# Performance work log

Measured on AMD Instinct MI355X. Metric: run time of the kernel, lower is better.

Reference implementation:

```python
import jax, jax.numpy as jnp
import numpy as np

B, IN, OUT, LAT = 8192, 256, 256, 128

def setup_inputs() -> dict:
    key = jax.random.key(0)
    ks = jax.random.split(key, 6)
    s = 0.05
    return {
        "x": jax.random.normal(ks[0], (B, IN), dtype=jnp.float32),
        "latent": jax.random.normal(ks[1], (B, LAT), dtype=jnp.float32),
        "Ww": jax.random.normal(ks[2], (LAT, IN * OUT), dtype=jnp.float32) * s,
        "bw": jax.random.normal(ks[3], (IN * OUT,), dtype=jnp.float32) * s,
        "Wb": jax.random.normal(ks[4], (LAT, OUT), dtype=jnp.float32) * s,
        "bb": jax.random.normal(ks[5], (OUT,), dtype=jnp.float32) * s,
    }

def reference(x, latent, Ww, bw, Wb, bb):
    lead = x.shape[:-1]
    x2 = x.reshape(-1, x.shape[-1])            # [B, in]
    l2 = latent.reshape(-1, latent.shape[-1])  # [B, lat]
    # per-sample weight: [B, in, out]
    weight = (l2 @ Ww + bw).reshape(-1, IN, OUT)
    # per-sample bias: [B, out]
    bias = l2 @ Wb + bb
    out = jnp.einsum('bi,bio->bo', x2, weight) + bias
    return out.reshape(*lead, OUT)
```

## Files before the change

### kernel.cpp

```cpp
#include <hip/hip_runtime.h>
#include <cstdint>
#include <cstddef>

#define BATCH  8192
#define IN_N   256
#define OUT_N  256
#define LAT_N  128
#define SLABS  129
#define KT     (SLABS * IN_N)
#define KT16   (KT / 16)
#define SPLITK 4

typedef _Float16 h8 __attribute__((ext_vector_type(8)));
typedef _Float16 h4 __attribute__((ext_vector_type(4)));
typedef float    f16v __attribute__((ext_vector_type(16)));
typedef float    f4v  __attribute__((ext_vector_type(4)));

#define WS_BP    0
#define WS_XH    16908288
#define WS_LT    21102592
#define WS_PARTS 23216128

__global__ void k_transpose(const float* __restrict__ Ww, const float* __restrict__ bw,
                            _Float16* __restrict__ Bp) {
    __shared__ float tile[64][65];
    const int k0 = blockIdx.x * 64;
    const int o0 = blockIdx.y * 64;
    const int t  = threadIdx.x;
    const int c  = t & 63, r0 = t >> 6;
#pragma unroll
    for (int j = 0; j < 16; ++j) {
        int r = r0 + 4 * j;
        int k = k0 + r;
        float v;
        if (k < LAT_N * IN_N) v = Ww[(size_t)k * 256 + o0 + c];
        else                  v = bw[(size_t)(k - LAT_N * IN_N) * 256 + o0 + c];
        tile[r][c] = v;
    }
    __syncthreads();
    const int tl = t & 31, st = t >> 5;
    const int kt_l = st >> 1, nt_l = st & 1;
    const int nt   = blockIdx.y * 2 + nt_l;
    const int kt16 = blockIdx.x * 4 + kt_l;
    _Float16* dst = Bp + ((size_t)(nt * KT16 + kt16) * 64) * 8;
#pragma unroll
    for (int kh = 0; kh < 2; ++kh) {
        h8 v;
#pragma unroll
        for (int h = 0; h < 8; ++h)
            v[h] = (_Float16)tile[kt_l * 16 + kh * 8 + h][nt_l * 32 + tl];
        *(h8*)(dst + (size_t)(kh * 32 + tl) * 8) = v;
    }
}

__global__ void k_convert(const float* __restrict__ x, const float* __restrict__ latent,
                          _Float16* __restrict__ Xh, _Float16* __restrict__ LT) {
    const int bid = blockIdx.x;
    if (bid < 2048) {
        int i = (bid * 256 + threadIdx.x) * 4;
        float4 v = *(const float4*)(x + i);
        h4 o;
        o[0] = (_Float16)v.x; o[1] = (_Float16)v.y;
        o[2] = (_Float16)v.z; o[3] = (_Float16)v.w;
        *(h4*)(Xh + i) = o;
    } else if (bid < 2048 + 4096) {
        int i = (bid - 2048) * 256 + threadIdx.x;
        int b = i >> 7, l = i & 127;
        LT[(size_t)l * BATCH + b] = (_Float16)latent[i];
    } else {
        int b = (bid - 2048 - 4096) * 256 + threadIdx.x;
        LT[(size_t)LAT_N * BATCH + b] = (_Float16)1.0f;
    }
}

__global__ void k_bias(const float* __restrict__ latent, const float* __restrict__ Wb,
                       const float* __restrict__ bb, float* __restrict__ part0) {
    __shared__ float lat[8][128];
    const int b0 = blockIdx.x * 8;
    const int t = threadIdx.x;
#pragma unroll
    for (int j = 0; j < 4; ++j) {
        int idx = t + 256 * j;
        int rr = idx >> 7, l = idx & 127;
        lat[rr][l] = latent[(size_t)(b0 + rr) * 128 + l];
    }
    __syncthreads();
    const int o = t;
    float acc[8];
    float bbv = bb[o];
#pragma unroll
    for (int rr = 0; rr < 8; ++rr) acc[rr] = bbv;
    for (int l = 0; l < 128; ++l) {
        float w = Wb[l * 256 + o];
#pragma unroll
        for (int rr = 0; rr < 8; ++rr) acc[rr] += lat[rr][l] * w;
    }
#pragma unroll
    for (int rr = 0; rr < 8; ++rr) part0[(size_t)(b0 + rr) * 256 + o] = acc[rr];
}

__global__ __launch_bounds__(256, 2) void k_gemm(const _Float16* __restrict__ Bp,
                                                 const _Float16* __restrict__ Xh,
                                                 const _Float16* __restrict__ LT,
                                                 float* __restrict__ parts) {
    __shared__ _Float16 Xs[64 * 256];

    const int bid   = blockIdx.x;
    const int m_blk = bid >> 2;
    const int ks    = bid & 3;
    const int m0    = m_blk * 64;
    const int slab0 = (ks == 0) ? 0 : 33 + 32 * (ks - 1);
    const int nslab = (ks == 0) ? 33 : 32;

    const int tid = threadIdx.x, wid = tid >> 6, lane = tid & 63;
    const int l32 = lane & 31, khalf = lane >> 5;

    for (int j = 0; j < 8; ++j) {
        int G = j * 256 + tid;
        int m = G >> 5, gp = G & 31;
        int g = gp ^ (m & 7);
        h8 v = *(const h8*)(Xh + (size_t)(m0 + m) * IN_N + g * 8);
        *(h8*)(Xs + m * IN_N + gp * 8) = v;
    }
    __syncthreads();

    int mrow[2], m7[2], pbase[2], m6[2];
#pragma unroll
    for (int t = 0; t < 2; ++t) {
        mrow[t]  = t * 32 + l32;
        m7[t]    = mrow[t] & 7;
        m6[t]    = m7[t] & 6;
        pbase[t] = mrow[t] * IN_N + (khalf ^ (m7[t] & 1)) * 8;
    }

    const _Float16* ltp = LT + (size_t)slab0 * BATCH + m0;
    _Float16 s_cur[2], s_nxt[2];
#pragma unroll
    for (int t = 0; t < 2; ++t) s_cur[t] = ltp[mrow[t]];

    const _Float16* bp0 = Bp + ((size_t)((wid * 2 + 0) * KT16 + slab0 * 16) * 64 + lane) * 8;
    const _Float16* bp1 = Bp + ((size_t)((wid * 2 + 1) * KT16 + slab0 * 16) * 64 + lane) * 8;

    f16v acc[2][2];
#pragma unroll
    for (int t = 0; t < 2; ++t)
#pragma unroll
        for (int u = 0; u < 2; ++u)
#pragma unroll
            for (int r = 0; r < 16; ++r) acc[t][u][r] = 0.0f;

    for (int sl = 0; sl < nslab; ++sl) {
        if (sl) {
#pragma unroll
            for (int t = 0; t < 2; ++t) s_cur[t] = s_nxt[t];
        }
        if (sl + 1 < nslab) {
            const _Float16* p = ltp + (size_t)(sl + 1) * BATCH;
#pragma unroll
            for (int t = 0; t < 2; ++t) s_nxt[t] = p[mrow[t]];
        }
        h8 s8[2];
#pragma unroll
        for (int t = 0; t < 2; ++t) {
            _Float16 s = s_cur[t];
            s8[t][0]=s; s8[t][1]=s; s8[t][2]=s; s8[t][3]=s;
            s8[t][4]=s; s8[t][5]=s; s8[t][6]=s; s8[t][7]=s;
        }
        const _Float16* b0p = bp0 + (size_t)sl * (16 * 512);
        const _Float16* b1p = bp1 + (size_t)sl * (16 * 512);
#pragma unroll
        for (int ks16 = 0; ks16 < 16; ++ks16) {
            h8 b0 = *(const h8*)(b0p + ks16 * 512);
            h8 b1 = *(const h8*)(b1p + ks16 * 512);
            h8 a[2];
#pragma unroll
            for (int t = 0; t < 2; ++t) {
                int off = pbase[t] + ((ks16 * 2) ^ m6[t]) * 8;
                h8 xv = *(const h8*)(Xs + off);
                a[t] = xv * s8[t];
            }
#pragma unroll
            for (int t = 0; t < 2; ++t) {
                acc[t][0] = __builtin_amdgcn_mfma_f32_32x32x16_f16(a[t], b0, acc[t][0], 0, 0, 0);
                acc[t][1] = __builtin_amdgcn_mfma_f32_32x32x16_f16(a[t], b1, acc[t][1], 0, 0, 0);
            }
        }
    }

    float* dst = parts + (size_t)ks * ((size_t)BATCH * OUT_N);
#pragma unroll
    for (int t = 0; t < 2; ++t) {
        int rowb = m0 + t * 32;
#pragma unroll
        for (int u = 0; u < 2; ++u) {
            int col = wid * 64 + u * 32 + l32;
#pragma unroll
            for (int r = 0; r < 16; ++r) {
                int row = rowb + (r & 3) + 8 * (r >> 2) + 4 * khalf;
                size_t off = (size_t)row * OUT_N + col;
                float v = acc[t][u][r];
                if (ks == 0) dst[off] += v;
                else         dst[off] = v;
            }
        }
    }
}

__global__ void k_reduce(const float* __restrict__ parts, float* __restrict__ out) {
    int i = (blockIdx.x * 256 + threadIdx.x) * 4;
    f4v s = *(const f4v*)(parts + i);
    s += *(const f4v*)(parts + 2097152 + i);
    s += *(const f4v*)(parts + 2 * 2097152 + i);
    s += *(const f4v*)(parts + 3 * 2097152 + i);
    *(f4v*)(out + i) = s;
}

extern "C" void kernel_launch(void* const* d_in, const int* in_sizes, int n_in,
                              void* d_out, int out_size, void* d_ws, size_t ws_size,
                              hipStream_t stream) {
    const float* x      = (const float*)d_in[0];
    const float* latent = (const float*)d_in[1];
    const float* Ww     = (const float*)d_in[2];
    const float* bw     = (const float*)d_in[3];
    const float* Wb     = (const float*)d_in[4];
    const float* bb     = (const float*)d_in[5];

    char* ws = (char*)d_ws;
    _Float16* Bp    = (_Float16*)(ws + WS_BP);
    _Float16* Xh    = (_Float16*)(ws + WS_XH);
    _Float16* LT    = (_Float16*)(ws + WS_LT);
    float*    parts = (float*)(ws + WS_PARTS);
    float*    out   = (float*)d_out;

    k_transpose<<<dim3(516, 4), 256, 0, stream>>>(Ww, bw, Bp);
    k_convert<<<6176, 256, 0, stream>>>(x, latent, Xh, LT);
    k_bias<<<1024, 256, 0, stream>>>(latent, Wb, bb, parts + 0);
    k_gemm<<<512, 256, 0, stream>>>(Bp, Xh, LT, parts);
    k_reduce<<<2048, 256, 0, stream>>>(parts, out);
}
```

Before: 291.2 us.

## Merge prep kernels into one launch and widen GEMM blocks to 8 waves

Folds the weight transpose, input conversion and bias GEMV into a single k_prep launch whose blocks dispatch on their index, cutting the number of kernel launches and the gaps between them. The main GEMM now uses 512 threads (8 waves), and each wave computes one 32-wide N tile instead of two. This halves the accumulators per wave and raises the number of waves sharing the X tile held in shared memory. In exchange, each wave issues fewer MFMAs per A-fragment LDS read, so reuse of A per wave falls.

```diff
diff --git a/kernel.cpp b/kernel.cpp
--- a/kernel.cpp
+++ b/kernel.cpp
@@ -21,85 +21,91 @@
 #define WS_LT    21102592
 #define WS_PARTS 23216128
 
-__global__ void k_transpose(const float* __restrict__ Ww, const float* __restrict__ bw,
-                            _Float16* __restrict__ Bp) {
-    __shared__ float tile[64][65];
-    const int k0 = blockIdx.x * 64;
-    const int o0 = blockIdx.y * 64;
-    const int t  = threadIdx.x;
-    const int c  = t & 63, r0 = t >> 6;
-#pragma unroll
-    for (int j = 0; j < 16; ++j) {
-        int r = r0 + 4 * j;
-        int k = k0 + r;
-        float v;
-        if (k < LAT_N * IN_N) v = Ww[(size_t)k * 256 + o0 + c];
-        else                  v = bw[(size_t)(k - LAT_N * IN_N) * 256 + o0 + c];
-        tile[r][c] = v;
-    }
-    __syncthreads();
-    const int tl = t & 31, st = t >> 5;
-    const int kt_l = st >> 1, nt_l = st & 1;
-    const int nt   = blockIdx.y * 2 + nt_l;
-    const int kt16 = blockIdx.x * 4 + kt_l;
-    _Float16* dst = Bp + ((size_t)(nt * KT16 + kt16) * 64) * 8;
-#pragma unroll
-    for (int kh = 0; kh < 2; ++kh) {
-        h8 v;
-#pragma unroll
-        for (int h = 0; h < 8; ++h)
-            v[h] = (_Float16)tile[kt_l * 16 + kh * 8 + h][nt_l * 32 + tl];
-        *(h8*)(dst + (size_t)(kh * 32 + tl) * 8) = v;
-    }
-}
-
-__global__ void k_convert(const float* __restrict__ x, const float* __restrict__ latent,
-                          _Float16* __restrict__ Xh, _Float16* __restrict__ LT) {
+#define PREP_T0   0
+#define PREP_T1   2064
+#define PREP_C1   8240
+#define PREP_B1   9264
+__global__ void k_prep(const float* __restrict__ Ww, const float* __restrict__ bw,
+                       const float* __restrict__ x,  const float* __restrict__ latent,
+                       const float* __restrict__ Wb, const float* __restrict__ bb,
+                       _Float16* __restrict__ Bp, _Float16* __restrict__ Xh,
+                       _Float16* __restrict__ LT, float* __restrict__ part0) {
+    __shared__ float smem[64 * 65];
     const int bid = blockIdx.x;
-    if (bid < 2048) {
-        int i = (bid * 256 + threadIdx.x) * 4;
-        float4 v = *(const float4*)(x + i);
-        h4 o;
-        o[0] = (_Float16)v.x; o[1] = (_Float16)v.y;
-        o[2] = (_Float16)v.z; o[3] = (_Float16)v.w;
-        *(h4*)(Xh + i) = o;
-    } else if (bid < 2048 + 4096) {
-        int i = (bid - 2048) * 256 + threadIdx.x;
-        int b = i >> 7, l = i & 127;
-        LT[(size_t)l * BATCH + b] = (_Float16)latent[i];
+    const int t   = threadIdx.x;
+
+    if (bid < PREP_T1) {
+        const int kx = bid % 516, oy = bid / 516;
+        const int k0 = kx * 64;
+        const int o0 = oy * 64;
+        const int c  = t & 63, r0 = t >> 6;
+        float (*tile)[65] = (float(*)[65])smem;
+#pragma unroll
+        for (int j = 0; j < 16; ++j) {
+            int r = r0 + 4 * j;
+            int k = k0 + r;
+            float v;
+            if (k < LAT_N * IN_N) v = Ww[(size_t)k * 256 + o0 + c];
+            else                  v = bw[(size_t)(k - LAT_N * IN_N) * 256 + o0 + c];
+            tile[r][c] = v;
+        }
+        __syncthreads();
+        const int tl = t & 31, st = t >> 5;
+        const int kt_l = st >> 1, nt_l = st & 1;
+        const int nt   = oy * 2 + nt_l;
+        const int kt16 = kx * 4 + kt_l;
+        _Float16* dst = Bp + ((size_t)(nt * KT16 + kt16) * 64) * 8;
+#pragma unroll
+        for (int kh = 0; kh < 2; ++kh) {
+            h8 v;
+#pragma unroll
+            for (int h = 0; h < 8; ++h)
+                v[h] = (_Float16)tile[kt_l * 16 + kh * 8 + h][nt_l * 32 + tl];
+            *(h8*)(dst + (size_t)(kh * 32 + tl) * 8) = v;
+        }
+    } else if (bid < PREP_C1) {
+        const int cb = bid - PREP_T1;
+        if (cb < 2048) {
+            int i = (cb * 256 + t) * 4;
+            float4 v = *(const float4*)(x + i);
+            h4 o;
+            o[0] = (_Float16)v.x; o[1] = (_Float16)v.y;
+            o[2] = (_Float16)v.z; o[3] = (_Float16)v.w;
+            *(h4*)(Xh + i) = o;
+        } else if (cb < 2048 + 4096) {
+            int i = (cb - 2048) * 256 + t;
+            int b = i >> 7, l = i & 127;
+            LT[(size_t)l * BATCH + b] = (_Float16)latent[i];
+        } else {
+            int b = (cb - 2048 - 4096) * 256 + t;
+            LT[(size_t)LAT_N * BATCH + b] = (_Float16)1.0f;
+        }
     } else {
-        int b = (bid - 2048 - 4096) * 256 + threadIdx.x;
-        LT[(size_t)LAT_N * BATCH + b] = (_Float16)1.0f;
-    }
-}
-
-__global__ void k_bias(const float* __restrict__ latent, const float* __restrict__ Wb,
-                       const float* __restrict__ bb, float* __restrict__ part0) {
-    __shared__ float lat[8][128];
-    const int b0 = blockIdx.x * 8;
-    const int t = threadIdx.x;
-#pragma unroll
-    for (int j = 0; j < 4; ++j) {
-        int idx = t + 256 * j;
-        int rr = idx >> 7, l = idx & 127;
-        lat[rr][l] = latent[(size_t)(b0 + rr) * 128 + l];
-    }
-    __syncthreads();
-    const int o = t;
-    float acc[8];
-    float bbv = bb[o];
-#pragma unroll
-    for (int rr = 0; rr < 8; ++rr) acc[rr] = bbv;
-    for (int l = 0; l < 128; ++l) {
-        float w = Wb[l * 256 + o];
-#pragma unroll
-        for (int rr = 0; rr < 8; ++rr) acc[rr] += lat[rr][l] * w;
-    }
-#pragma unroll
-    for (int rr = 0; rr < 8; ++rr) part0[(size_t)(b0 + rr) * 256 + o] = acc[rr];
-}
-
-__global__ __launch_bounds__(256, 2) void k_gemm(const _Float16* __restrict__ Bp,
+        float (*lat)[128] = (float(*)[128])smem;
+        const int b0 = (bid - PREP_C1) * 8;
+#pragma unroll
+        for (int j = 0; j < 4; ++j) {
+            int idx = t + 256 * j;
+            int rr = idx >> 7, l = idx & 127;
+            lat[rr][l] = latent[(size_t)(b0 + rr) * 128 + l];
+        }
+        __syncthreads();
+        const int o = t;
+        float acc[8];
+        float bbv = bb[o];
+#pragma unroll
+        for (int rr = 0; rr < 8; ++rr) acc[rr] = bbv;
+        for (int l = 0; l < 128; ++l) {
+            float w = Wb[l * 256 + o];
+#pragma unroll
+            for (int rr = 0; rr < 8; ++rr) acc[rr] += lat[rr][l] * w;
+        }
+#pragma unroll
+        for (int rr = 0; rr < 8; ++rr) part0[(size_t)(b0 + rr) * 256 + o] = acc[rr];
+    }
+}
+
+__global__ __launch_bounds__(512, 4) void k_gemm(const _Float16* __restrict__ Bp,
                                                  const _Float16* __restrict__ Xh,
                                                  const _Float16* __restrict__ LT,
                                                  float* __restrict__ parts) {
@@ -115,8 +121,8 @@
     const int tid = threadIdx.x, wid = tid >> 6, lane = tid & 63;
     const int l32 = lane & 31, khalf = lane >> 5;
 
-    for (int j = 0; j < 8; ++j) {
-        int G = j * 256 + tid;
+    for (int j = 0; j < 4; ++j) {
+        int G = j * 512 + tid;
         int m = G >> 5, gp = G & 31;
         int g = gp ^ (m & 7);
         h8 v = *(const h8*)(Xh + (size_t)(m0 + m) * IN_N + g * 8);
@@ -138,16 +144,13 @@
 #pragma unroll
     for (int t = 0; t < 2; ++t) s_cur[t] = ltp[mrow[t]];
 
-    const _Float16* bp0 = Bp + ((size_t)((wid * 2 + 0) * KT16 + slab0 * 16) * 64 + lane) * 8;
-    const _Float16* bp1 = Bp + ((size_t)((wid * 2 + 1) * KT16 + slab0 * 16) * 64 + lane) * 8;
-
-    f16v acc[2][2];
+    const _Float16* bp = Bp + ((size_t)(wid * KT16 + slab0 * 16) * 64 + lane) * 8;
+
+    f16v acc[2];
 #pragma unroll
     for (int t = 0; t < 2; ++t)
 #pragma unroll
-        for (int u = 0; u < 2; ++u)
-#pragma unroll
-            for (int r = 0; r < 16; ++r) acc[t][u][r] = 0.0f;
+        for (int r = 0; r < 16; ++r) acc[t][r] = 0.0f;
 
     for (int sl = 0; sl < nslab; ++sl) {
         if (sl) {
@@ -166,12 +169,10 @@
             s8[t][0]=s; s8[t][1]=s; s8[t][2]=s; s8[t][3]=s;
             s8[t][4]=s; s8[t][5]=s; s8[t][6]=s; s8[t][7]=s;
         }
-        const _Float16* b0p = bp0 + (size_t)sl * (16 * 512);
-        const _Float16* b1p = bp1 + (size_t)sl * (16 * 512);
+        const _Float16* bsl = bp + (size_t)sl * (16 * 512);
 #pragma unroll
         for (int ks16 = 0; ks16 < 16; ++ks16) {
-            h8 b0 = *(const h8*)(b0p + ks16 * 512);
-            h8 b1 = *(const h8*)(b1p + ks16 * 512);
+            h8 b = *(const h8*)(bsl + ks16 * 512);
             h8 a[2];
 #pragma unroll
             for (int t = 0; t < 2; ++t) {
@@ -180,10 +181,8 @@
                 a[t] = xv * s8[t];
             }
 #pragma unroll
-            for (int t = 0; t < 2; ++t) {
-                acc[t][0] = __builtin_amdgcn_mfma_f32_32x32x16_f16(a[t], b0, acc[t][0], 0, 0, 0);
-                acc[t][1] = __builtin_amdgcn_mfma_f32_32x32x16_f16(a[t], b1, acc[t][1], 0, 0, 0);
-            }
+            for (int t = 0; t < 2; ++t)
+                acc[t] = __builtin_amdgcn_mfma_f32_32x32x16_f16(a[t], b, acc[t], 0, 0, 0);
         }
     }
 
@@ -191,17 +190,14 @@
 #pragma unroll
     for (int t = 0; t < 2; ++t) {
         int rowb = m0 + t * 32;
-#pragma unroll
-        for (int u = 0; u < 2; ++u) {
-            int col = wid * 64 + u * 32 + l32;
-#pragma unroll
-            for (int r = 0; r < 16; ++r) {
-                int row = rowb + (r & 3) + 8 * (r >> 2) + 4 * khalf;
-                size_t off = (size_t)row * OUT_N + col;
-                float v = acc[t][u][r];
-                if (ks == 0) dst[off] += v;
-                else         dst[off] = v;
-            }
+        int col  = wid * 32 + l32;
+#pragma unroll
+        for (int r = 0; r < 16; ++r) {
+            int row = rowb + (r & 3) + 8 * (r >> 2) + 4 * khalf;
+            size_t off = (size_t)row * OUT_N + col;
+            float v = acc[t][r];
+            if (ks == 0) dst[off] += v;
+            else         dst[off] = v;
         }
     }
 }
@@ -232,9 +228,7 @@
     float*    parts = (float*)(ws + WS_PARTS);
     float*    out   = (float*)d_out;
 
-    k_transpose<<<dim3(516, 4), 256, 0, stream>>>(Ww, bw, Bp);
-    k_convert<<<6176, 256, 0, stream>>>(x, latent, Xh, LT);
-    k_bias<<<1024, 256, 0, stream>>>(latent, Wb, bb, parts + 0);
-    k_gemm<<<512, 256, 0, stream>>>(Bp, Xh, LT, parts);
+    k_prep<<<PREP_B1, 256, 0, stream>>>(Ww, bw, x, latent, Wb, bb, Bp, Xh, LT, parts);
+    k_gemm<<<512, 512, 0, stream>>>(Bp, Xh, LT, parts);
     k_reduce<<<2048, 256, 0, stream>>>(parts, out);
 }
```

Result: slower. 453.5 us (+55.7%).

## Fuse weight transpose, input conversion and bias GEMM into one prep kernel

Applied to the files above, without the earlier changes.

Merges the three preprocessing kernels (weight transpose to fp16 MFMA layout, x/latent conversion, per-sample bias) into a single launch that dispatches on block ID. The weight transpose now converts to fp16 before staging in shared memory, covering a full 64x256 tile per block with float4 loads. The latent transpose goes through a shared-memory tile so the LT writes are coalesced instead of strided scalar stores, and the x conversion and ones row use wider vector stores. This removes two launch gaps and the uncoalesced writes, at the cost of a larger shared-memory footprint per block that can limit occupancy.

```diff
diff --git a/kernel.cpp b/kernel.cpp
--- a/kernel.cpp
+++ b/kernel.cpp
@@ -13,6 +13,7 @@
 
 typedef _Float16 h8 __attribute__((ext_vector_type(8)));
 typedef _Float16 h4 __attribute__((ext_vector_type(4)));
+typedef _Float16 h2 __attribute__((ext_vector_type(2)));
 typedef float    f16v __attribute__((ext_vector_type(16)));
 typedef float    f4v  __attribute__((ext_vector_type(4)));
 
@@ -21,82 +22,118 @@
 #define WS_LT    21102592
 #define WS_PARTS 23216128
 
-__global__ void k_transpose(const float* __restrict__ Ww, const float* __restrict__ bw,
-                            _Float16* __restrict__ Bp) {
-    __shared__ float tile[64][65];
-    const int k0 = blockIdx.x * 64;
-    const int o0 = blockIdx.y * 64;
-    const int t  = threadIdx.x;
-    const int c  = t & 63, r0 = t >> 6;
-#pragma unroll
-    for (int j = 0; j < 16; ++j) {
-        int r = r0 + 4 * j;
-        int k = k0 + r;
-        float v;
-        if (k < LAT_N * IN_N) v = Ww[(size_t)k * 256 + o0 + c];
-        else                  v = bw[(size_t)(k - LAT_N * IN_N) * 256 + o0 + c];
-        tile[r][c] = v;
-    }
-    __syncthreads();
-    const int tl = t & 31, st = t >> 5;
-    const int kt_l = st >> 1, nt_l = st & 1;
-    const int nt   = blockIdx.y * 2 + nt_l;
-    const int kt16 = blockIdx.x * 4 + kt_l;
-    _Float16* dst = Bp + ((size_t)(nt * KT16 + kt16) * 64) * 8;
-#pragma unroll
-    for (int kh = 0; kh < 2; ++kh) {
-        h8 v;
-#pragma unroll
-        for (int h = 0; h < 8; ++h)
-            v[h] = (_Float16)tile[kt_l * 16 + kh * 8 + h][nt_l * 32 + tl];
-        *(h8*)(dst + (size_t)(kh * 32 + tl) * 8) = v;
-    }
-}
-
-__global__ void k_convert(const float* __restrict__ x, const float* __restrict__ latent,
-                          _Float16* __restrict__ Xh, _Float16* __restrict__ LT) {
+#define PR_T1   516
+#define PR_L1   580
+#define PR_X1   1604
+#define PR_O1   1608
+#define PR_B1   2632
+__global__ void k_prep(const float* __restrict__ Ww, const float* __restrict__ bw,
+                       const float* __restrict__ x,  const float* __restrict__ latent,
+                       const float* __restrict__ Wb, const float* __restrict__ bb,
+                       _Float16* __restrict__ Bp, _Float16* __restrict__ Xh,
+                       _Float16* __restrict__ LT, float* __restrict__ part0) {
+    __shared__ _Float16 smemh[16512];
     const int bid = blockIdx.x;
-    if (bid < 2048) {
-        int i = (bid * 256 + threadIdx.x) * 4;
-        float4 v = *(const float4*)(x + i);
-        h4 o;
-        o[0] = (_Float16)v.x; o[1] = (_Float16)v.y;
-        o[2] = (_Float16)v.z; o[3] = (_Float16)v.w;
-        *(h4*)(Xh + i) = o;
-    } else if (bid < 2048 + 4096) {
-        int i = (bid - 2048) * 256 + threadIdx.x;
-        int b = i >> 7, l = i & 127;
-        LT[(size_t)l * BATCH + b] = (_Float16)latent[i];
+    const int t   = threadIdx.x;
+
+    if (bid < PR_T1) {
+        _Float16* tile = smemh;
+        const int k0 = bid * 64;
+#pragma unroll
+        for (int j = 0; j < 16; ++j) {
+            int idx = j * 256 + t;
+            int row = idx >> 6, col = (idx & 63) * 4;
+            int k = k0 + row;
+            const float* src = (k < LAT_N * IN_N)
+                             ? Ww + (size_t)k * 256 + col
+                             : bw + (size_t)(k - LAT_N * IN_N) * 256 + col;
+            float4 v = *(const float4*)src;
+            h4 o;
+            o[0] = (_Float16)v.x; o[1] = (_Float16)v.y;
+            o[2] = (_Float16)v.z; o[3] = (_Float16)v.w;
+            *(h4*)(tile + row * 256 + col) = o;
+        }
+        __syncthreads();
+        const int tl = t & 31;
+#pragma unroll
+        for (int j = 0; j < 4; ++j) {
+            int stid = j * 8 + (t >> 5);
+            int kt_l = stid >> 3, nt = stid & 7;
+            int kt16 = bid * 4 + kt_l;
+            _Float16* dst = Bp + ((size_t)(nt * KT16 + kt16) * 64) * 8;
+#pragma unroll
+            for (int kh = 0; kh < 2; ++kh) {
+                h8 v;
+#pragma unroll
+                for (int h = 0; h < 8; ++h)
+                    v[h] = tile[(kt_l * 16 + kh * 8 + h) * 256 + nt * 32 + tl];
+                *(h8*)(dst + (size_t)(kh * 32 + tl) * 8) = v;
+            }
+        }
+    } else if (bid < PR_L1) {
+        _Float16* t2 = smemh;
+        const int b0 = (bid - PR_T1) * 128;
+#pragma unroll
+        for (int j = 0; j < 16; ++j) {
+            int idx = j * 256 + t;
+            int b = idx >> 5, l = (idx & 31) * 4;
+            float4 v = *(const float4*)(latent + (size_t)(b0 + b) * 128 + l);
+            t2[(l + 0) * 129 + b] = (_Float16)v.x;
+            t2[(l + 1) * 129 + b] = (_Float16)v.y;
+            t2[(l + 2) * 129 + b] = (_Float16)v.z;
+            t2[(l + 3) * 129 + b] = (_Float16)v.w;
+        }
+        __syncthreads();
+#pragma unroll
+        for (int j = 0; j < 32; ++j) {
+            int idx = j * 256 + t;
+            int l = idx >> 6, bb = (idx & 63) * 2;
+            h2 w;
+            w[0] = t2[l * 129 + bb];
+            w[1] = t2[l * 129 + bb + 1];
+            *(h2*)(LT + (size_t)l * BATCH + b0 + bb) = w;
+        }
+    } else if (bid < PR_X1) {
+        const int cb = bid - PR_L1;
+        int i = (cb * 256 + t) * 8;
+        float4 v0 = *(const float4*)(x + i);
+        float4 v1 = *(const float4*)(x + i + 4);
+        h8 o;
+        o[0] = (_Float16)v0.x; o[1] = (_Float16)v0.y;
+        o[2] = (_Float16)v0.z; o[3] = (_Float16)v0.w;
+        o[4] = (_Float16)v1.x; o[5] = (_Float16)v1.y;
+        o[6] = (_Float16)v1.z; o[7] = (_Float16)v1.w;
+        *(h8*)(Xh + i) = o;
+    } else if (bid < PR_O1) {
+        const int ob = bid - PR_X1;
+        int base = ob * 2048 + t * 8;
+        h8 o;
+#pragma unroll
+        for (int h = 0; h < 8; ++h) o[h] = (_Float16)1.0f;
+        *(h8*)(LT + (size_t)LAT_N * BATCH + base) = o;
     } else {
-        int b = (bid - 2048 - 4096) * 256 + threadIdx.x;
-        LT[(size_t)LAT_N * BATCH + b] = (_Float16)1.0f;
-    }
-}
-
-__global__ void k_bias(const float* __restrict__ latent, const float* __restrict__ Wb,
-                       const float* __restrict__ bb, float* __restrict__ part0) {
-    __shared__ float lat[8][128];
-    const int b0 = blockIdx.x * 8;
-    const int t = threadIdx.x;
-#pragma unroll
-    for (int j = 0; j < 4; ++j) {
-        int idx = t + 256 * j;
-        int rr = idx >> 7, l = idx & 127;
-        lat[rr][l] = latent[(size_t)(b0 + rr) * 128 + l];
-    }
-    __syncthreads();
-    const int o = t;
-    float acc[8];
-    float bbv = bb[o];
-#pragma unroll
-    for (int rr = 0; rr < 8; ++rr) acc[rr] = bbv;
-    for (int l = 0; l < 128; ++l) {
-        float w = Wb[l * 256 + o];
-#pragma unroll
-        for (int rr = 0; rr < 8; ++rr) acc[rr] += lat[rr][l] * w;
-    }
-#pragma unroll
-    for (int rr = 0; rr < 8; ++rr) part0[(size_t)(b0 + rr) * 256 + o] = acc[rr];
+        float* lat = (float*)smemh;
+        const int b0 = (bid - PR_O1) * 8;
+#pragma unroll
+        for (int j = 0; j < 4; ++j) {
+            int idx = t + 256 * j;
+            int rr = idx >> 7, l = idx & 127;
+            lat[rr * 128 + l] = latent[(size_t)(b0 + rr) * 128 + l];
+        }
+        __syncthreads();
+        const int o = t;
+        float acc[8];
+        float bbv = bb[o];
+#pragma unroll
+        for (int rr = 0; rr < 8; ++rr) acc[rr] = bbv;
+        for (int l = 0; l < 128; ++l) {
+            float w = Wb[l * 256 + o];
+#pragma unroll
+            for (int rr = 0; rr < 8; ++rr) acc[rr] += lat[rr * 128 + l] * w;
+        }
+#pragma unroll
+        for (int rr = 0; rr < 8; ++rr) part0[(size_t)(b0 + rr) * 256 + o] = acc[rr];
+    }
 }
 
 __global__ __launch_bounds__(256, 2) void k_gemm(const _Float16* __restrict__ Bp,
@@ -232,9 +269,7 @@
     float*    parts = (float*)(ws + WS_PARTS);
     float*    out   = (float*)d_out;
 
-    k_transpose<<<dim3(516, 4), 256, 0, stream>>>(Ww, bw, Bp);
-    k_convert<<<6176, 256, 0, stream>>>(x, latent, Xh, LT);
-    k_bias<<<1024, 256, 0, stream>>>(latent, Wb, bb, parts + 0);
+    k_prep<<<PR_B1, 256, 0, stream>>>(Ww, bw, x, latent, Wb, bb, Bp, Xh, LT, parts);
     k_gemm<<<512, 256, 0, stream>>>(Bp, Xh, LT, parts);
     k_reduce<<<2048, 256, 0, stream>>>(parts, out);
 }
```

Result: faster. 273.1 us (-6.2%).
